# Optimization experiments

Measured on AMD Instinct MI355X. Metric: run time of the kernel, lower is better.

## Reference

```python
import jax, jax.numpy as jnp
from jax import lax
import numpy as np

N = 60000   # total nodes
B = 8       # graphs in batch
GS = N // B # nodes per graph
F = 384     # input node features
E = 600000  # edges
H = 6       # hiddenSize (hardcoded in source)
C = 10      # num_classes


def setup_inputs() -> dict:
    key = jax.random.key(0)
    ks = jax.random.split(key, 8)
    x = jax.random.normal(ks[0], (N, F), jnp.float32)
    src = jax.random.randint(ks[1], (E,), 0, N, jnp.int32)
    off = jax.random.randint(ks[2], (E,), 1, GS, jnp.int32)  # 1..GS-1 -> no self loops
    dst = (src // GS) * GS + (src % GS + off) % GS           # same-graph endpoint
    batch = jnp.arange(N, dtype=jnp.int32) // GS
    W1 = jax.random.normal(ks[3], (F, H), jnp.float32) * (1.0 / np.sqrt(F))
    b1 = jnp.zeros((H,), jnp.float32)
    W2 = jax.random.normal(ks[4], (H, C), jnp.float32) * (1.0 / np.sqrt(H))
    b2 = jnp.zeros((C,), jnp.float32)
    Wp1 = jax.random.normal(ks[5], (2 * H,), jnp.float32) * (1.0 / np.sqrt(2 * H))
    bp1 = jnp.zeros((), jnp.float32)
    Wp2 = jax.random.normal(ks[6], (2 * C,), jnp.float32) * (1.0 / np.sqrt(2 * C))
    bp2 = jnp.zeros((), jnp.float32)
    return dict(x=x, src=src, dst=dst, batch=batch, W1=W1, b1=b1, W2=W2, b2=b2,
                Wp1=Wp1, bp1=bp1, Wp2=Wp2, bp2=bp2)


def gcn_conv(x, src, dst, evalid, nvalid, W, b):
    # PyG GCNConv: h = x W; add remaining self-loops (weight 1); deg over dst;
    # norm = dinv[src]*dinv[dst]; aggregate to dst; + bias.
    n = x.shape[0]
    h = x @ W
    ef = evalid.astype(h.dtype)
    is_loop = evalid & (src == dst)
    has_loop = jax.ops.segment_sum(is_loop.astype(jnp.int32), dst, num_segments=n) > 0
    add_loop = (nvalid & ~has_loop).astype(h.dtype)
    deg = jax.ops.segment_sum(ef, dst, num_segments=n) + add_loop
    dinv = jnp.where(deg > 0, lax.rsqrt(jnp.maximum(deg, 1e-12)), 0.0)
    coef = ef * dinv[src] * dinv[dst]
    out = jax.ops.segment_sum(h[src] * coef[:, None], dst, num_segments=n)
    out = out + (add_loop * dinv * dinv)[:, None] * h
    return out + b


def edge_pool(x, src, dst, evalid, nvalid, Wp, bp):
    # PyG EdgePooling: raw = lin([x_src||x_dst]); score = softmax(raw, dst) + 0.5;
    # greedy contraction of edges by descending score; new_x = (sum over cluster) * score.
    n, f = x.shape
    raw = x[src] @ Wp[:f] + x[dst] @ Wp[f:] + bp                      # [E]
    rm = jnp.where(evalid, raw, -jnp.inf)
    m = jax.ops.segment_max(rm, dst, num_segments=n)
    m = jnp.where(jnp.isfinite(m), m, 0.0)
    ex = jnp.where(evalid, jnp.exp(raw - m[dst]), 0.0)
    s = jax.ops.segment_sum(ex, dst, num_segments=n)
    score = jnp.where(evalid, ex / jnp.where(s[dst] > 0, s[dst], 1.0), 0.0) + 0.5

    order = jnp.argsort(jnp.where(evalid, -score, jnp.inf))           # descending, invalid last

    def step(rem, edg):
        s_, d_, v_ = edg
        take = v_ & rem[s_] & rem[d_]
        rem = rem.at[s_].set(rem[s_] & ~take)
        rem = rem.at[d_].set(rem[d_] & ~take)
        return rem, take

    _, chosen_sorted = lax.scan(step, nvalid, (src[order], dst[order], evalid[order]))
    chosen = jnp.zeros_like(evalid).at[order].set(chosen_sorted)

    chf = chosen.astype(x.dtype)
    nonself = src != dst
    dead = jax.ops.segment_sum((chosen & nonself).astype(jnp.int32), dst, num_segments=n) > 0
    new_valid = nvalid & ~dead

    # merged feature: (x_src + x_dst) * score at slot src; unmatched: x * 1
    added = jnp.zeros_like(x).at[src].add((chf * nonself.astype(x.dtype))[:, None] * x[dst])
    scale = 1.0 + jnp.zeros((n,), x.dtype).at[src].add(chf * (score - 1.0))
    new_x = jnp.where(new_valid[:, None], (x + added) * scale[:, None], 0.0)

    # cluster map (dst of chosen edge -> src slot), remap + coalesce (dedup) edges
    merged_src = jnp.full((n,), -1, jnp.int32).at[dst].max(jnp.where(chosen, src, -1))
    cmap = jnp.where(merged_src >= 0, merged_src, jnp.arange(n, dtype=jnp.int32))
    ns, nd = cmap[src], cmap[dst]
    ns_k = jnp.where(evalid, ns, n)  # push invalid edges to the end
    order2 = jnp.lexsort((nd, ns_k))
    ss, dd = ns_k[order2], nd[order2]
    diff = (ss[1:] != ss[:-1]) | (dd[1:] != dd[:-1])
    first = jnp.concatenate([jnp.ones((1,), bool), diff])
    new_evalid = jnp.zeros_like(evalid).at[order2].set(first & evalid[order2])
    return new_x, ns, nd, new_evalid, new_valid


def _forward(x, src, dst, batch, W1, b1, W2, b2, Wp1, bp1, Wp2, bp2):
    evalid = jnp.ones((src.shape[0],), bool)
    nvalid = jnp.ones((x.shape[0],), bool)
    h = jax.nn.relu(gcn_conv(x, src, dst, evalid, nvalid, W1, b1))
    # dropout: identity in eval mode
    h, s1, d1, ev1, nv1 = edge_pool(h, src, dst, evalid, nvalid, Wp1, bp1)
    h = gcn_conv(h, s1, d1, ev1, nv1, W2, b2)
    h, s2, d2, ev2, nv2 = edge_pool(h, s1, d1, ev1, nv1, Wp2, bp2)
    nvf = nv2.astype(h.dtype)
    cnt = jax.ops.segment_sum(nvf, batch, num_segments=B)
    sm = jax.ops.segment_sum(h * nvf[:, None], batch, num_segments=B)
    g = sm / cnt[:, None]
    return jax.nn.log_softmax(g, axis=1)


def reference(x, src, dst, batch, W1, b1, W2, b2, Wp1, bp1, Wp2, bp2):
    return _forward(x, src, dst, batch, W1, b1, W2, b2, Wp1, bp1, Wp2, bp2)
```

## Files before the change

kernel.cpp:

```cpp
#include <hip/hip_runtime.h>
#include <math.h>

#define NN 60000
#define BB 8
#define GS 7500
#define FF 384
#define EE 600000
#define HH 6
#define CC 10
#define HT_BITS 20
#define HT_SIZE (1u << HT_BITS)
#define HT_MASK (HT_SIZE - 1u)
#define TPB 256
#define CAP 80000
#define REMW ((GS + 31) / 32)
#define GPAD 32
#define SCAN_B 1024
#define NBLK ((NN + SCAN_B - 1) / SCAN_B)
static_assert(NBLK <= 64, "scan3 wave-scan assumes <=64 blocks");
static_assert((HH % 2) == 0 && (CC % 2) == 0, "float2 paths assume even fd");

static inline int ngrid(int n) { return (n + TPB - 1) / TPB; }

__device__ __forceinline__ unsigned long long mkprio(float sc, int e) {
  return (((unsigned long long)__float_as_uint(sc)) << 32) |
         (unsigned int)(~(unsigned int)e);
}

__global__ void k_mm1(const float* __restrict__ x, const float* __restrict__ W,
                      float* __restrict__ out) {
  __shared__ float Ws[FF * HH];
  for (int i = threadIdx.x; i < FF * HH; i += blockDim.x) Ws[i] = W[i];
  __syncthreads();
  int wave = threadIdx.x >> 6, lane = threadIdx.x & 63;
  int node = blockIdx.x * 4 + wave;
  if (node >= NN) return;
  const float* xr = x + (size_t)node * FF;
  float acc[HH] = {0.f, 0.f, 0.f, 0.f, 0.f, 0.f};
  for (int k = lane; k < FF; k += 64) {
    float xv = xr[k];
#pragma unroll
    for (int j = 0; j < HH; j++) acc[j] += xv * Ws[k * HH + j];
  }
#pragma unroll
  for (int j = 0; j < HH; j++) {
#pragma unroll
    for (int o = 32; o > 0; o >>= 1) acc[j] += __shfl_down(acc[j], o, 64);
  }
  if (lane == 0) {
#pragma unroll
    for (int j = 0; j < HH; j++) out[(size_t)node * HH + j] = acc[j];
  }
}

__global__ void k_prep(float* __restrict__ deg, unsigned char* __restrict__ hasloop,
                       int* __restrict__ gcntsA,
                       int* __restrict__ gcntsB, float* __restrict__ gsum,
                       float* __restrict__ gcnt, const unsigned char* __restrict__ nvin,
                       unsigned char* __restrict__ nvout, float* __restrict__ scale,
                       int* __restrict__ merged, int* __restrict__ partner,
                       unsigned long long* __restrict__ bestA,
                       unsigned long long* __restrict__ bestB,
                       unsigned char* __restrict__ remG) {
  int v = blockIdx.x * blockDim.x + threadIdx.x;
  if (v >= NN) return;
  deg[v] = 0.f;
  hasloop[v] = 0;
  unsigned char nvv = nvin ? nvin[v] : 1;
  nvout[v] = nvv;
  remG[v] = nvv;
  bestA[v] = 0ULL;
  bestB[v] = 0ULL;
  scale[v] = 1.0f;
  if (merged) merged[v] = -1;
  partner[v] = -1;
  if (v < BB * GPAD) { gcntsA[v] = 0; gcntsB[v] = 0; }
  if (v < BB * CC) gsum[v] = 0.f;
  if (v < BB) gcnt[v] = 0.f;
}

__global__ void k_deg(const int* __restrict__ src, const int* __restrict__ dst,
                      const unsigned char* __restrict__ ev, float* __restrict__ deg,
                      unsigned char* __restrict__ hasloop) {
  int e = blockIdx.x * blockDim.x + threadIdx.x;
  if (e >= EE) return;
  if (ev && !ev[e]) return;
  int d = dst[e];
  atomicAdd(&deg[d], 1.0f);
  if (src[e] == d) hasloop[d] = 1;
}

__global__ __launch_bounds__(1024) void k_scan1(const float* __restrict__ deg,
                                                int* __restrict__ rowstart,
                                                int* __restrict__ bsum) {
  __shared__ int tmp[SCAN_B];
  int t = threadIdx.x;
  int i = blockIdx.x * SCAN_B + t;
  int v = (i < NN) ? (int)deg[i] : 0;
  tmp[t] = v;
  __syncthreads();
  for (int o = 1; o < SCAN_B; o <<= 1) {
    int y = (t >= o) ? tmp[t - o] : 0;
    __syncthreads();
    tmp[t] += y;
    __syncthreads();
  }
  if (i < NN) rowstart[i] = tmp[t] - v;
  if (t == SCAN_B - 1) bsum[blockIdx.x] = tmp[t];
}

__global__ void k_scan3(int* __restrict__ rowstart, const int* __restrict__ bsum,
                        int* __restrict__ fill, const float* __restrict__ deg,
                        const unsigned char* __restrict__ hasloop,
                        const unsigned char* __restrict__ nv, float* __restrict__ dinv,
                        unsigned char* __restrict__ addloop) {
  __shared__ int offs[64];
  __shared__ int total;
  int t = threadIdx.x;
  if (t < 64) {
    int v = (t < NBLK) ? bsum[t] : 0;
    int x = v;
#pragma unroll
    for (int o = 1; o < 64; o <<= 1) {
      int y = __shfl_up(x, o, 64);
      if (t >= o) x += y;
    }
    offs[t] = x - v;
    if (t == 63) total = x;
  }
  __syncthreads();
  int i = blockIdx.x * blockDim.x + t;
  if (i >= NN) return;
  int r = rowstart[i] + offs[i >> 10];
  rowstart[i] = r;
  fill[i] = r;
  if (i == NN - 1) rowstart[NN] = total;
  int nvv = nv ? (int)nv[i] : 1;
  unsigned char al = (nvv && !hasloop[i]) ? 1 : 0;
  float d = deg[i] + (float)al;
  dinv[i] = d > 0.f ? 1.0f / sqrtf(fmaxf(d, 1e-12f)) : 0.f;
  addloop[i] = al;
}

__global__ void k_scatter(const int* __restrict__ src, const int* __restrict__ dst,
                          const unsigned char* __restrict__ ev, int* __restrict__ fill,
                          int* __restrict__ csrS, int* __restrict__ csrE) {
  int e = blockIdx.x * blockDim.x + threadIdx.x;
  if (e >= EE) return;
  if (ev && !ev[e]) return;
  int d = dst[e];
  int p = atomicAdd(&fill[d], 1);
  csrS[p] = src[e];
  csrE[p] = e;
}

template <int FD>
__global__ void k_agg_fin(const int* __restrict__ rowstart, const int* __restrict__ csrS,
                          const float* __restrict__ dinv, const unsigned char* __restrict__ addloop,
                          const float* __restrict__ h, const float* __restrict__ b,
                          float* __restrict__ out, int relu) {
  int v = blockIdx.x * blockDim.x + threadIdx.x;
  if (v >= NN) return;
  int b0 = rowstart[v], b1 = rowstart[v + 1];
  float acc[FD];
#pragma unroll
  for (int j = 0; j < FD; j++) acc[j] = 0.f;
  float dv = dinv[v];
  for (int i = b0; i < b1; i++) {
    int s = csrS[i];
    float c = dinv[s] * dv;
    const float2* hr2 = (const float2*)(h + (size_t)s * FD);
#pragma unroll
    for (int j = 0; j < FD / 2; j++) {
      float2 hv = hr2[j];
      acc[2 * j] += hv.x * c;
      acc[2 * j + 1] += hv.y * c;
    }
  }
  float cl = addloop[v] ? dv * dv : 0.f;
  const float* hv = h + (size_t)v * FD;
#pragma unroll
  for (int j = 0; j < FD; j++) {
    float o = acc[j] + cl * hv[j] + b[j];
    if (relu) o = fmaxf(o, 0.f);
    out[(size_t)v * FD + j] = o;
  }
}

__global__ void k_raw(const float* __restrict__ x, const int* __restrict__ src,
                      const int* __restrict__ dst, const unsigned char* __restrict__ ev,
                      const float* __restrict__ Wp, const float* __restrict__ bp,
                      float* __restrict__ raw, unsigned char* __restrict__ chosen, int fd) {
  int e = blockIdx.x * blockDim.x + threadIdx.x;
  if (e >= EE) return;
  chosen[e] = 0;
  if (ev && !ev[e]) return;
  int s = src[e], d = dst[e];
  float r = bp[0];
  const float2* xs = (const float2*)(x + (size_t)s * fd);
  const float2* xd = (const float2*)(x + (size_t)d * fd);
  int h2 = fd >> 1;
  for (int j = 0; j < h2; j++) {
    float2 v = xs[j];
    r += v.x * Wp[2 * j];
    r += v.y * Wp[2 * j + 1];
  }
  for (int j = 0; j < h2; j++) {
    float2 v = xd[j];
    r += v.x * Wp[fd + 2 * j];
    r += v.y * Wp[fd + 2 * j + 1];
  }
  raw[e] = r;
}

__global__ void k_smscore(const int* __restrict__ rowstart, const int* __restrict__ csrS,
                          const int* __restrict__ csrE, const float* __restrict__ raw,
                          const unsigned char* __restrict__ remG, float* __restrict__ score,
                          unsigned long long* __restrict__ bestA) {
  int v = blockIdx.x * blockDim.x + threadIdx.x;
  if (v >= NN) return;
  int b0 = rowstart[v], b1 = rowstart[v + 1];
  if (b0 == b1) return;
  float m = -INFINITY;
  for (int i = b0; i < b1; i++) m = fmaxf(m, raw[csrE[i]]);
  float s = 0.f;
  for (int i = b0; i < b1; i++) s += expf(raw[csrE[i]] - m);
  if (!remG[v]) return;
  float sd = s > 0.f ? s : 1.0f;
  unsigned long long lb = 0ULL;
  for (int i = b0; i < b1; i++) {
    int sv = csrS[i];
    if (!remG[sv]) continue;
    int e = csrE[i];
    float sc = expf(raw[e] - m) / sd + 0.5f;
    score[e] = sc;
    unsigned long long p = mkprio(sc, e);
    if (p > lb) lb = p;
    if (sv != v && p > bestA[sv]) atomicMax(&bestA[sv], p);
  }
  if (lb > bestA[v]) atomicMax(&bestA[v], lb);
}

__global__ void k_r1sel(const int* __restrict__ src, const int* __restrict__ dst,
                        const float* __restrict__ score, const unsigned char* __restrict__ ev,
                        unsigned char* __restrict__ remG,
                        const unsigned long long* __restrict__ bestA,
                        unsigned long long* __restrict__ bestB,
                        unsigned char* __restrict__ chosen, ulonglong2* __restrict__ recs,
                        int* __restrict__ gcnts) {
  __shared__ int wcnt[TPB / 64][BB];
  __shared__ int bbase[BB];
  int e = blockIdx.x * blockDim.x + threadIdx.x;
  int w = threadIdx.x >> 6, lane = threadIdx.x & 63;
  int keep = 0, s = 0, d = 0, g = 0;
  unsigned long long p = 0;
  if (e < EE && (!ev || ev[e])) {
    s = src[e];
    d = dst[e];
    g = s / GS;
    if (remG[s] && remG[d]) {
      p = mkprio(score[e], e);
      if (bestA[s] == p && bestA[d] == p) {
        chosen[e] = 1;
        remG[s] = 0;
        remG[d] = 0;
      } else {
        keep = 1;
        bestB[s] = 0ULL;
        bestB[d] = 0ULL;
      }
    }
  }
  int myrank = 0;
#pragma unroll
  for (int gg = 0; gg < BB; gg++) {
    unsigned long long m = __ballot(keep && g == gg);
    if (keep && g == gg) myrank = __popcll(m & ((1ULL << lane) - 1ULL));
    if (lane == 0) wcnt[w][gg] = __popcll(m);
  }
  __syncthreads();
  if (threadIdx.x < BB) {
    int gg = threadIdx.x, tot = 0;
#pragma unroll
    for (int ww = 0; ww < TPB / 64; ww++) {
      int c = wcnt[ww][gg];
      wcnt[ww][gg] = tot;
      tot += c;
    }
    bbase[gg] = tot ? atomicAdd(&gcnts[gg * GPAD], tot) : 0;
  }
  __syncthreads();
  if (keep)
    recs[(size_t)g * CAP + bbase[g] + wcnt[w][g] + myrank] =
        make_ulonglong2(p, (((unsigned long long)(unsigned int)s) << 32) | (unsigned int)d);
}

__global__ void k_gpost(const ulonglong2* __restrict__ recs, const int* __restrict__ gcnts,
                        const unsigned char* __restrict__ remG,
                        unsigned long long* __restrict__ bestC, int* __restrict__ gcntsOut) {
  int g = blockIdx.y;
  if (blockIdx.x == 0 && threadIdx.x == 0) gcntsOut[g * GPAD] = 0;
  int n = gcnts[g * GPAD];
  const ulonglong2* lst = recs + (size_t)g * CAP;
  int stride = gridDim.x * blockDim.x;
  for (int i = blockIdx.x * blockDim.x + threadIdx.x; i < n; i += stride) {
    ulonglong2 r = lst[i];
    int s = (int)(r.y >> 32), d = (int)(r.y & 0xFFFFFFFFu);
    if (remG[s] && remG[d]) {
      if (r.x > bestC[s]) atomicMax(&bestC[s], r.x);
      if (d != s && r.x > bestC[d]) atomicMax(&bestC[d], r.x);
    }
  }
}

__global__ void k_gsel(const ulonglong2* __restrict__ recsIn, const int* __restrict__ gcntsIn,
                       unsigned char* __restrict__ remG,
                       const unsigned long long* __restrict__ bestC,
                       unsigned long long* __restrict__ bestN,
                       unsigned char* __restrict__ chosen, ulonglong2* __restrict__ recsOut,
                       int* __restrict__ gcntsOut) {
  int g = blockIdx.y;
  int n = gcntsIn[g * GPAD];
  const ulonglong2* lst = recsIn + (size_t)g * CAP;
  ulonglong2* outl = recsOut + (size_t)g * CAP;
  int lane = threadIdx.x & 63;
  int stride = gridDim.x * blockDim.x;
  for (int i = blockIdx.x * blockDim.x + threadIdx.x; i - lane < n; i += stride) {
    int keep = 0;
    ulonglong2 r;
    if (i < n) {
      r = lst[i];
      int s = (int)(r.y >> 32), d = (int)(r.y & 0xFFFFFFFFu);
      if (remG[s] && remG[d]) {
        if (bestC[s] == r.x && bestC[d] == r.x) {
          int e = (int)(~(unsigned int)(r.x & 0xFFFFFFFFu));
          chosen[e] = 1;
          remG[s] = 0;
          remG[d] = 0;
        } else {
          keep = 1;
          bestN[s] = 0ULL;
          bestN[d] = 0ULL;
        }
      }
    }
    unsigned long long m = __ballot(keep);
    int tot = __popcll(m);
    int pre = __popcll(m & ((1ULL << lane) - 1ULL));
    int b0 = 0;
    if (lane == 0 && tot) b0 = atomicAdd(&gcntsOut[g * GPAD], tot);
    b0 = __shfl(b0, 0, 64);
    if (keep) outl[b0 + pre] = r;
  }
}

__global__ __launch_bounds__(1024) void k_match_g(ulonglong2* __restrict__ recs0,
                                                  ulonglong2* __restrict__ recs1,
                                                  const int* __restrict__ gcnts,
                                                  const unsigned char* __restrict__ remG,
                                                  unsigned char* __restrict__ chosen) {
  __shared__ unsigned long long best[GS];
  __shared__ unsigned int remB[REMW];
  __shared__ int cnt_next;
  const int g = blockIdx.x;
  const int base = g * GS;
  const int t = threadIdx.x, nth = blockDim.x;
  const int lane = t & 63;

  for (int w = t; w < REMW; w += nth) {
    unsigned int bits = 0;
    int v0 = w * 32;
    if (v0 + 32 <= GS) {
      const unsigned int* p4 = (const unsigned int*)(remG + base + v0);
#pragma unroll
      for (int q = 0; q < 8; q++) {
        unsigned int x4 = p4[q];
        bits |= ((x4 & 1u) << (q * 4)) | (((x4 >> 8) & 1u) << (q * 4 + 1)) |
                (((x4 >> 16) & 1u) << (q * 4 + 2)) | (((x4 >> 24) & 1u) << (q * 4 + 3));
      }
    } else {
      for (int b = 0; b < 32; b++) {
        int v = v0 + b;
        if (v < GS) bits |= (remG[base + v] ? 1u : 0u) << b;
      }
    }
    remB[w] = bits;
  }
  for (int i = t; i < GS; i += nth) best[i] = 0ULL;
  __syncthreads();

  ulonglong2* bufs[2] = {recs0 + (size_t)g * CAP, recs1 + (size_t)g * CAP};
  int n = gcnts[g * GPAD];
  int cur = 0;
  int guard = 0;

  while (n > 0) {
    if (++guard > 100000) break;
    for (int i0 = 0; i0 < n; i0 += nth * 4) {
      ulonglong2 r[4];
      int have[4];
#pragma unroll
      for (int k = 0; k < 4; k++) {
        int i = i0 + t + k * nth;
        have[k] = i < n;
        if (have[k]) r[k] = bufs[cur][i];
      }
#pragma unroll
      for (int k = 0; k < 4; k++) {
        if (!have[k]) continue;
        int ls = (int)(r[k].y >> 32) - base, ld = (int)(r[k].y & 0xFFFFFFFFu) - base;
        if (((remB[ls >> 5] >> (ls & 31)) & 1u) && ((remB[ld >> 5] >> (ld & 31)) & 1u)) {
          atomicMax(&best[ls], r[k].x);
          if (ld != ls) atomicMax(&best[ld], r[k].x);
        }
      }
    }
    if (t == 0) cnt_next = 0;
    __syncthreads();
    for (int i0 = 0; i0 < n; i0 += nth * 4) {
      ulonglong2 r[4];
      int have[4];
#pragma unroll
      for (int k = 0; k < 4; k++) {
        int i = i0 + t + k * nth;
        have[k] = i < n;
        if (have[k]) r[k] = bufs[cur][i];
      }
#pragma unroll
      for (int k = 0; k < 4; k++) {
        int keep = 0;
        int ls = 0, ld = 0;
        if (have[k]) {
          ls = (int)(r[k].y >> 32) - base;
          ld = (int)(r[k].y & 0xFFFFFFFFu) - base;
          if (((remB[ls >> 5] >> (ls & 31)) & 1u) && ((remB[ld >> 5] >> (ld & 31)) & 1u)) {
            if (best[ls] == r[k].x && best[ld] == r[k].x) {
              int e = (int)(~(unsigned int)(r[k].x & 0xFFFFFFFFu));
              chosen[e] = 1;
              atomicAnd(&remB[ls >> 5], ~(1u << (ls & 31)));
              atomicAnd(&remB[ld >> 5], ~(1u << (ld & 31)));
            } else {
              keep = 1;
            }
          }
        }
        unsigned long long m = __ballot(keep);
        int tot = __popcll(m);
        int pre = __popcll(m & ((1ULL << lane) - 1ULL));
        int b0 = 0;
        if (lane == 0 && tot) b0 = atomicAdd(&cnt_next, tot);
        b0 = __shfl(b0, 0, 64);
        if (keep) bufs[cur ^ 1][b0 + pre] = r[k];
      }
    }
    __syncthreads();
    n = cnt_next;
    if (n < 4096) {
      for (int i = t; i < n; i += nth) {
        ulonglong2 r = bufs[cur ^ 1][i];
        best[(int)(r.y >> 32) - base] = 0ULL;
        best[(int)(r.y & 0xFFFFFFFFu) - base] = 0ULL;
      }
    } else {
      for (int i = t; i < GS; i += nth) best[i] = 0ULL;
    }
    __syncthreads();
    cur ^= 1;
  }
}

__global__ void k_pool_edge(const int* __restrict__ src, const int* __restrict__ dst,
                            const unsigned char* __restrict__ chosen, const float* __restrict__ score,
                            unsigned char* __restrict__ nvout, float* __restrict__ scale,
                            int* __restrict__ partner, int* __restrict__ merged) {
  int e = blockIdx.x * blockDim.x + threadIdx.x;
  if (e >= EE) return;
  if (!chosen[e]) return;
  int s = src[e], d = dst[e];
  scale[s] = score[e];
  if (merged) merged[d] = s;
  if (s != d) {
    nvout[d] = 0;
    partner[s] = d;
  }
}

__global__ void k_newx_mm2(const float* __restrict__ h1, const int* __restrict__ partner,
                           const float* __restrict__ scale, const unsigned char* __restrict__ nvout,
                           const float* __restrict__ W2, float* __restrict__ h2pre) {
  int v = blockIdx.x * blockDim.x + threadIdx.x;
  if (v >= NN) return;
  float sc = scale[v];
  int ok = nvout[v];
  int p = partner[v];
  float nx[HH];
#pragma unroll
  for (int j = 0; j < HH; j++) {
    float a = h1[(size_t)v * HH + j];
    if (p >= 0) a += h1[(size_t)p * HH + j];
    nx[j] = ok ? a * sc : 0.f;
  }
#pragma unroll
  for (int c = 0; c < CC; c++) {
    float a = 0.f;
#pragma unroll
    for (int j = 0; j < HH; j++) a += nx[j] * W2[j * CC + c];
    h2pre[(size_t)v * CC + c] = a;
  }
}

__device__ __forceinline__ unsigned int ht_hash(unsigned long long key) {
  return (unsigned int)((key * 0x9E3779B97F4A7C15ULL) >> 44) & HT_MASK;
}

__global__ void k_remap_ins(const int* __restrict__ src, const int* __restrict__ dst,
                            const int* __restrict__ merged, int* __restrict__ ns,
                            int* __restrict__ nd, unsigned long long* __restrict__ htab) {
  int e = blockIdx.x * blockDim.x + threadIdx.x;
  if (e >= EE) return;
  int s = src[e], d = dst[e];
  int ms = merged[s], md = merged[d];
  int a = ms >= 0 ? ms : s;
  int b = md >= 0 ? md : d;
  ns[e] = a;
  nd[e] = b;
  unsigned long long key =
      (unsigned long long)((((unsigned int)a) << 16) | (unsigned int)b);
  unsigned long long val = (key << 32) | (unsigned int)e;
  unsigned int h = ht_hash(key);
  for (;;) {
    unsigned long long curv = htab[h];
    if (curv == ~0ULL) {
      unsigned long long prev = atomicCAS(&htab[h], ~0ULL, val);
      if (prev == ~0ULL) break;
      curv = prev;
    }
    if ((curv >> 32) == key) {
      if ((curv & 0xFFFFFFFFULL) > (unsigned long long)(unsigned int)e)
        atomicMin(&htab[h], val);
      break;
    }
    h = (h + 1) & HT_MASK;
  }
}

__global__ void k_dedup_mark(const int* __restrict__ ns, const int* __restrict__ nd,
                             const unsigned long long* __restrict__ htab,
                             unsigned char* __restrict__ evout) {
  int e = blockIdx.x * blockDim.x + threadIdx.x;
  if (e >= EE) return;
  unsigned long long key =
      (unsigned long long)((((unsigned int)ns[e]) << 16) | (unsigned int)nd[e]);
  unsigned int h = ht_hash(key);
  for (;;) {
    unsigned long long curv = htab[h];
    if ((curv >> 32) == key) {
      evout[e] = ((curv & 0xFFFFFFFFULL) == (unsigned long long)(unsigned int)e) ? 1 : 0;
      return;
    }
    h = (h + 1) & HT_MASK;
  }
}

__global__ void k_newx_pool(const float* __restrict__ h2, const int* __restrict__ partner,
                            const float* __restrict__ scale, const unsigned char* __restrict__ nv,
                            float* __restrict__ gsum, float* __restrict__ gcnt) {
  int v = blockIdx.x * blockDim.x + threadIdx.x;
  int lane = threadIdx.x & 63;
  int b = (v < NN ? v : NN - 1) / GS;
  int active = (v < NN) && nv[v];
  float cnt = active ? 1.f : 0.f;
  float val[CC];
  if (active) {
    float sc = scale[v];
    int p = partner[v];
    for (int j = 0; j < CC; j++) {
      float a = h2[(size_t)v * CC + j];
      if (p >= 0) a += h2[(size_t)p * CC + j];
      val[j] = a * sc;
    }
  } else {
    for (int j = 0; j < CC; j++) val[j] = 0.f;
  }
  int b0 = __shfl(b, 0, 64);
  unsigned long long same = __ballot(b == b0);
  if (same == ~0ULL) {
    for (int o = 32; o > 0; o >>= 1) {
      cnt += __shfl_down(cnt, o, 64);
      for (int j = 0; j < CC; j++) val[j] += __shfl_down(val[j], o, 64);
    }
    if (lane == 0 && cnt > 0.f) {
      atomicAdd(&gcnt[b0], cnt);
      for (int j = 0; j < CC; j++) atomicAdd(&gsum[b0 * CC + j], val[j]);
    }
  } else if (active) {
    atomicAdd(&gcnt[b], cnt);
    for (int j = 0; j < CC; j++) atomicAdd(&gsum[b * CC + j], val[j]);
  }
}

__global__ void k_logsm(const float* __restrict__ gsum, const float* __restrict__ gcnt,
                        float* __restrict__ out) {
  int t = threadIdx.x;
  if (t >= BB) return;
  float gr[CC];
  float c = gcnt[t];
  float m = -INFINITY;
  for (int j = 0; j < CC; j++) {
    gr[j] = gsum[t * CC + j] / c;
    m = fmaxf(m, gr[j]);
  }
  float s = 0.f;
  for (int j = 0; j < CC; j++) s += expf(gr[j] - m);
  float l = logf(s);
  for (int j = 0; j < CC; j++) out[t * CC + j] = gr[j] - m - l;
}

extern "C" void kernel_launch(void* const* d_in, const int* in_sizes, int n_in,
                              void* d_out, int out_size, void* d_ws, size_t ws_size,
                              hipStream_t stream) {
  const float* x = (const float*)d_in[0];
  const int* src = (const int*)d_in[1];
  const int* dst = (const int*)d_in[2];
  const float* W1 = (const float*)d_in[4];
  const float* b1 = (const float*)d_in[5];
  const float* W2 = (const float*)d_in[6];
  const float* b2 = (const float*)d_in[7];
  const float* Wp1 = (const float*)d_in[8];
  const float* bp1 = (const float*)d_in[9];
  const float* Wp2 = (const float*)d_in[10];
  const float* bp2 = (const float*)d_in[11];
  float* out = (float*)d_out;

  char* wsb = (char*)d_ws;
  size_t off = 0;
  auto A = [&](size_t bytes) -> char* {
    char* r = wsb + off;
    off = (off + bytes + 255) & ~(size_t)255;
    return r;
  };
  float* h1pre = (float*)A((size_t)NN * HH * 4);
  float* h1out = (float*)A((size_t)NN * HH * 4);
  float* deg = (float*)A((size_t)NN * 4);
  float* dinv = (float*)A((size_t)NN * 4);
  unsigned char* hasloop = (unsigned char*)A(NN);
  unsigned char* addloop = (unsigned char*)A(NN);
  float* raw = (float*)A((size_t)EE * 4);
  float* score = (float*)A((size_t)EE * 4);
  unsigned char* chosen = (unsigned char*)A(EE);
  unsigned char* nv1 = (unsigned char*)A(NN);
  unsigned char* nv2 = (unsigned char*)A(NN);
  float* scale = (float*)A((size_t)NN * 4);
  int* partner = (int*)A((size_t)NN * 4);
  int* merged = (int*)A((size_t)NN * 4);
  int* ns = (int*)A((size_t)EE * 4);
  int* nd = (int*)A((size_t)EE * 4);
  unsigned char* ev1 = (unsigned char*)A(EE);
  unsigned long long* htab = (unsigned long long*)A((size_t)HT_SIZE * 8);
  float* h2pre = (float*)A((size_t)NN * CC * 4);
  float* h2out = (float*)A((size_t)NN * CC * 4);
  unsigned long long* bestA = (unsigned long long*)A((size_t)NN * 8);
  unsigned long long* bestB = (unsigned long long*)A((size_t)NN * 8);
  unsigned char* remG = (unsigned char*)A(NN);
  ulonglong2* recs0 = (ulonglong2*)A((size_t)BB * CAP * 16);
  ulonglong2* recs1 = (ulonglong2*)A((size_t)BB * CAP * 16);
  int* gcntsA = (int*)A((size_t)BB * GPAD * 4);
  int* gcntsB = (int*)A((size_t)BB * GPAD * 4);
  float* gsum = (float*)A((size_t)BB * CC * 4);
  float* gcnt = (float*)A((size_t)BB * 4);
  int* rowstart = (int*)A((size_t)(NN + 1) * 4);
  int* fill = (int*)A((size_t)NN * 4);
  int* bsum = (int*)A((size_t)64 * 4);
  int* csrS = (int*)A((size_t)EE * 4);
  int* csrE = (int*)A((size_t)EE * 4);
  (void)ws_size; (void)n_in; (void)in_sizes; (void)out_size;

  const int GE = ngrid(EE), GN = ngrid(NN);
  const dim3 RG(32, BB);

  hipMemsetAsync(htab, 0xFF, (size_t)HT_SIZE * 8, stream);
  hipLaunchKernelGGL(k_mm1, dim3((NN + 3) / 4), dim3(TPB), 0, stream, x, W1, h1pre);
  hipLaunchKernelGGL(k_prep, dim3(GN), dim3(TPB), 0, stream, deg, hasloop, gcntsA, gcntsB,
                     gsum, gcnt, (const unsigned char*)nullptr, nv1, scale, merged, partner, bestA, bestB, remG);
  hipLaunchKernelGGL(k_deg, dim3(GE), dim3(TPB), 0, stream, src, dst, (const unsigned char*)nullptr, deg, hasloop);
  hipLaunchKernelGGL(k_scan1, dim3(NBLK), dim3(SCAN_B), 0, stream, deg, rowstart, bsum);
  hipLaunchKernelGGL(k_scan3, dim3(GN), dim3(TPB), 0, stream, rowstart, bsum, fill, deg, hasloop,
                     (const unsigned char*)nullptr, dinv, addloop);
  hipLaunchKernelGGL(k_scatter, dim3(GE), dim3(TPB), 0, stream, src, dst, (const unsigned char*)nullptr, fill, csrS, csrE);
  hipLaunchKernelGGL(k_agg_fin<HH>, dim3(GN), dim3(TPB), 0, stream, rowstart, csrS, dinv, addloop, h1pre, b1, h1out, 1);

  hipLaunchKernelGGL(k_raw, dim3(GE), dim3(TPB), 0, stream, h1out, src, dst, (const unsigned char*)nullptr, Wp1, bp1, raw, chosen, HH);
  hipLaunchKernelGGL(k_smscore, dim3(GN), dim3(TPB), 0, stream, rowstart, csrS, csrE, raw, remG, score, bestA);
  hipLaunchKernelGGL(k_r1sel, dim3(GE), dim3(TPB), 0, stream, src, dst, score, (const unsigned char*)nullptr, remG, bestA, bestB, chosen, recs0, gcntsA);
  hipLaunchKernelGGL(k_gpost, RG, dim3(TPB), 0, stream, recs0, gcntsA, remG, bestB, gcntsB);
  hipLaunchKernelGGL(k_gsel, RG, dim3(TPB), 0, stream, recs0, gcntsA, remG, bestB, bestA, chosen, recs1, gcntsB);
  hipLaunchKernelGGL(k_gpost, RG, dim3(TPB), 0, stream, recs1, gcntsB, remG, bestA, gcntsA);
  hipLaunchKernelGGL(k_gsel, RG, dim3(TPB), 0, stream, recs1, gcntsB, remG, bestA, bestB, chosen, recs0, gcntsA);
  hipLaunchKernelGGL(k_gpost, RG, dim3(TPB), 0, stream, recs0, gcntsA, remG, bestB, gcntsB);
  hipLaunchKernelGGL(k_gsel, RG, dim3(TPB), 0, stream, recs0, gcntsA, remG, bestB, bestA, chosen, recs1, gcntsB);
  hipLaunchKernelGGL(k_gpost, RG, dim3(TPB), 0, stream, recs1, gcntsB, remG, bestA, gcntsA);
  hipLaunchKernelGGL(k_gsel, RG, dim3(TPB), 0, stream, recs1, gcntsB, remG, bestA, bestB, chosen, recs0, gcntsA);
  hipLaunchKernelGGL(k_gpost, RG, dim3(TPB), 0, stream, recs0, gcntsA, remG, bestB, gcntsB);
  hipLaunchKernelGGL(k_gsel, RG, dim3(TPB), 0, stream, recs0, gcntsA, remG, bestB, bestA, chosen, recs1, gcntsB);
  hipLaunchKernelGGL(k_match_g, dim3(BB), dim3(1024), 0, stream, recs1, recs0, gcntsB, remG, chosen);
  hipLaunchKernelGGL(k_pool_edge, dim3(GE), dim3(TPB), 0, stream, src, dst, chosen, score, nv1, scale, partner, merged);
  hipLaunchKernelGGL(k_newx_mm2, dim3(GN), dim3(TPB), 0, stream, h1out, partner, scale, nv1, W2, h2pre);
  hipLaunchKernelGGL(k_remap_ins, dim3(GE), dim3(TPB), 0, stream, src, dst, merged, ns, nd, htab);
  hipLaunchKernelGGL(k_dedup_mark, dim3(GE), dim3(TPB), 0, stream, ns, nd, htab, ev1);

  hipLaunchKernelGGL(k_prep, dim3(GN), dim3(TPB), 0, stream, deg, hasloop, gcntsA, gcntsB,
                     gsum, gcnt, (const unsigned char*)nv1, nv2, scale, (int*)nullptr, partner, bestA, bestB, remG);
  hipLaunchKernelGGL(k_deg, dim3(GE), dim3(TPB), 0, stream, ns, nd, (const unsigned char*)ev1, deg, hasloop);
  hipLaunchKernelGGL(k_scan1, dim3(NBLK), dim3(SCAN_B), 0, stream, deg, rowstart, bsum);
  hipLaunchKernelGGL(k_scan3, dim3(GN), dim3(TPB), 0, stream, rowstart, bsum, fill, deg, hasloop,
                     (const unsigned char*)nv1, dinv, addloop);
  hipLaunchKernelGGL(k_scatter, dim3(GE), dim3(TPB), 0, stream, ns, nd, (const unsigned char*)ev1, fill, csrS, csrE);
  hipLaunchKernelGGL(k_agg_fin<CC>, dim3(GN), dim3(TPB), 0, stream, rowstart, csrS, dinv, addloop, h2pre, b2, h2out, 0);

  hipLaunchKernelGGL(k_raw, dim3(GE), dim3(TPB), 0, stream, h2out, ns, nd, (const unsigned char*)ev1, Wp2, bp2, raw, chosen, CC);
  hipLaunchKernelGGL(k_smscore, dim3(GN), dim3(TPB), 0, stream, rowstart, csrS, csrE, raw, remG, score, bestA);
  hipLaunchKernelGGL(k_r1sel, dim3(GE), dim3(TPB), 0, stream, ns, nd, score, (const unsigned char*)ev1, remG, bestA, bestB, chosen, recs0, gcntsA);
  hipLaunchKernelGGL(k_gpost, RG, dim3(TPB), 0, stream, recs0, gcntsA, remG, bestB, gcntsB);
  hipLaunchKernelGGL(k_gsel, RG, dim3(TPB), 0, stream, recs0, gcntsA, remG, bestB, bestA, chosen, recs1, gcntsB);
  hipLaunchKernelGGL(k_gpost, RG, dim3(TPB), 0, stream, recs1, gcntsB, remG, bestA, gcntsA);
  hipLaunchKernelGGL(k_gsel, RG, dim3(TPB), 0, stream, recs1, gcntsB, remG, bestA, bestB, chosen, recs0, gcntsA);
  hipLaunchKernelGGL(k_gpost, RG, dim3(TPB), 0, stream, recs0, gcntsA, remG, bestB, gcntsB);
  hipLaunchKernelGGL(k_gsel, RG, dim3(TPB), 0, stream, recs0, gcntsA, remG, bestB, bestA, chosen, recs1, gcntsB);
  hipLaunchKernelGGL(k_gpost, RG, dim3(TPB), 0, stream, recs1, gcntsB, remG, bestA, gcntsA);
  hipLaunchKernelGGL(k_gsel, RG, dim3(TPB), 0, stream, recs1, gcntsB, remG, bestA, bestB, chosen, recs0, gcntsA);
  hipLaunchKernelGGL(k_gpost, RG, dim3(TPB), 0, stream, recs0, gcntsA, remG, bestB, gcntsB);
  hipLaunchKernelGGL(k_gsel, RG, dim3(TPB), 0, stream, recs0, gcntsA, remG, bestB, bestA, chosen, recs1, gcntsB);
  hipLaunchKernelGGL(k_match_g, dim3(BB), dim3(1024), 0, stream, recs1, recs0, gcntsB, remG, chosen);
  hipLaunchKernelGGL(k_pool_edge, dim3(GE), dim3(TPB), 0, stream, ns, nd, chosen, score, nv2, scale, partner, (int*)nullptr);

  hipLaunchKernelGGL(k_newx_pool, dim3(GN), dim3(TPB), 0, stream, h2out, partner, scale, nv2, gsum, gcnt);
  hipLaunchKernelGGL(k_logsm, dim3(1), dim3(64), 0, stream, gsum, gcnt, out);
}
```

Before: 1.404 ms.

## Fuse iterative matching rounds into one cooperative kernel with grid syncs

Replaces the ten alternating k_gpost/k_gsel launches per pooling stage with a single cooperative kernel. It runs five rounds and separates the atomicMax phase from the select/compact phase with grid.sync(). The aim is to remove the per-launch overhead and inter-kernel gaps of twenty small launches. In exchange it adds grid-wide barrier cost and requires the 256-block grid to be co-resident for the cooperative launch.

```diff
diff --git a/kernel.cpp b/kernel.cpp
--- a/kernel.cpp
+++ b/kernel.cpp
@@ -1,5 +1,8 @@
 #include <hip/hip_runtime.h>
+#include <hip/hip_cooperative_groups.h>
 #include <math.h>
+
+namespace cg = cooperative_groups;
 
 #define NN 60000
 #define BB 8
@@ -295,62 +298,68 @@
         make_ulonglong2(p, (((unsigned long long)(unsigned int)s) << 32) | (unsigned int)d);
 }
 
-__global__ void k_gpost(const ulonglong2* __restrict__ recs, const int* __restrict__ gcnts,
-                        const unsigned char* __restrict__ remG,
-                        unsigned long long* __restrict__ bestC, int* __restrict__ gcntsOut) {
-  int g = blockIdx.y;
-  if (blockIdx.x == 0 && threadIdx.x == 0) gcntsOut[g * GPAD] = 0;
-  int n = gcnts[g * GPAD];
-  const ulonglong2* lst = recs + (size_t)g * CAP;
-  int stride = gridDim.x * blockDim.x;
-  for (int i = blockIdx.x * blockDim.x + threadIdx.x; i < n; i += stride) {
-    ulonglong2 r = lst[i];
-    int s = (int)(r.y >> 32), d = (int)(r.y & 0xFFFFFFFFu);
-    if (remG[s] && remG[d]) {
-      if (r.x > bestC[s]) atomicMax(&bestC[s], r.x);
-      if (d != s && r.x > bestC[d]) atomicMax(&bestC[d], r.x);
-    }
-  }
-}
-
-__global__ void k_gsel(const ulonglong2* __restrict__ recsIn, const int* __restrict__ gcntsIn,
-                       unsigned char* __restrict__ remG,
-                       const unsigned long long* __restrict__ bestC,
-                       unsigned long long* __restrict__ bestN,
-                       unsigned char* __restrict__ chosen, ulonglong2* __restrict__ recsOut,
-                       int* __restrict__ gcntsOut) {
-  int g = blockIdx.y;
-  int n = gcntsIn[g * GPAD];
-  const ulonglong2* lst = recsIn + (size_t)g * CAP;
-  ulonglong2* outl = recsOut + (size_t)g * CAP;
-  int lane = threadIdx.x & 63;
-  int stride = gridDim.x * blockDim.x;
-  for (int i = blockIdx.x * blockDim.x + threadIdx.x; i - lane < n; i += stride) {
-    int keep = 0;
-    ulonglong2 r;
-    if (i < n) {
-      r = lst[i];
-      int s = (int)(r.y >> 32), d = (int)(r.y & 0xFFFFFFFFu);
+__global__ void k_grounds(ulonglong2* __restrict__ recs0, ulonglong2* __restrict__ recs1,
+                          int* __restrict__ gcA, int* __restrict__ gcB,
+                          unsigned char* __restrict__ remG,
+                          unsigned long long* __restrict__ bestA,
+                          unsigned long long* __restrict__ bestB,
+                          unsigned char* __restrict__ chosen, int nrounds) {
+  cg::grid_group grid = cg::this_grid();
+  const int g = blockIdx.y;
+  const int lane = threadIdx.x & 63;
+  const int stride = gridDim.x * blockDim.x;
+  ulonglong2* rin = recs0;
+  ulonglong2* rout = recs1;
+  int* cin = gcA;
+  int* cout = gcB;
+  unsigned long long* bcur = bestB;
+  unsigned long long* bnext = bestA;
+
+  for (int r = 0; r < nrounds; r++) {
+    if (blockIdx.x == 0 && threadIdx.x == 0) cout[g * GPAD] = 0;
+    int n = cin[g * GPAD];
+    const ulonglong2* lst = rin + (size_t)g * CAP;
+    for (int i = blockIdx.x * blockDim.x + threadIdx.x; i < n; i += stride) {
+      ulonglong2 rr = lst[i];
+      int s = (int)(rr.y >> 32), d = (int)(rr.y & 0xFFFFFFFFu);
       if (remG[s] && remG[d]) {
-        if (bestC[s] == r.x && bestC[d] == r.x) {
-          int e = (int)(~(unsigned int)(r.x & 0xFFFFFFFFu));
-          chosen[e] = 1;
-          remG[s] = 0;
-          remG[d] = 0;
-        } else {
-          keep = 1;
-          bestN[s] = 0ULL;
-          bestN[d] = 0ULL;
+        if (rr.x > bcur[s]) atomicMax(&bcur[s], rr.x);
+        if (d != s && rr.x > bcur[d]) atomicMax(&bcur[d], rr.x);
+      }
+    }
+    grid.sync();
+    ulonglong2* outl = rout + (size_t)g * CAP;
+    for (int i = blockIdx.x * blockDim.x + threadIdx.x; i - lane < n; i += stride) {
+      int keep = 0;
+      ulonglong2 rr;
+      if (i < n) {
+        rr = lst[i];
+        int s = (int)(rr.y >> 32), d = (int)(rr.y & 0xFFFFFFFFu);
+        if (remG[s] && remG[d]) {
+          if (bcur[s] == rr.x && bcur[d] == rr.x) {
+            int e = (int)(~(unsigned int)(rr.x & 0xFFFFFFFFu));
+            chosen[e] = 1;
+            remG[s] = 0;
+            remG[d] = 0;
+          } else {
+            keep = 1;
+            bnext[s] = 0ULL;
+            bnext[d] = 0ULL;
+          }
         }
       }
-    }
-    unsigned long long m = __ballot(keep);
-    int tot = __popcll(m);
-    int pre = __popcll(m & ((1ULL << lane) - 1ULL));
-    int b0 = 0;
-    if (lane == 0 && tot) b0 = atomicAdd(&gcntsOut[g * GPAD], tot);
-    b0 = __shfl(b0, 0, 64);
-    if (keep) outl[b0 + pre] = r;
+      unsigned long long m = __ballot(keep);
+      int tot = __popcll(m);
+      int pre = __popcll(m & ((1ULL << lane) - 1ULL));
+      int b0 = 0;
+      if (lane == 0 && tot) b0 = atomicAdd(&cout[g * GPAD], tot);
+      b0 = __shfl(b0, 0, 64);
+      if (keep) outl[b0 + pre] = rr;
+    }
+    grid.sync();
+    ulonglong2* tr = rin; rin = rout; rout = tr;
+    int* tc = cin; cin = cout; cout = tc;
+    unsigned long long* tb = bcur; bcur = bnext; bnext = tb;
   }
 }
 
@@ -677,6 +686,8 @@
 
   const int GE = ngrid(EE), GN = ngrid(NN);
   const dim3 RG(32, BB);
+  int nrounds = 5;
+  void* gargs[] = {&recs0, &recs1, &gcntsA, &gcntsB, &remG, &bestA, &bestB, &chosen, &nrounds};
 
   hipMemsetAsync(htab, 0xFF, (size_t)HT_SIZE * 8, stream);
   hipLaunchKernelGGL(k_mm1, dim3((NN + 3) / 4), dim3(TPB), 0, stream, x, W1, h1pre);
@@ -692,16 +703,7 @@
   hipLaunchKernelGGL(k_raw, dim3(GE), dim3(TPB), 0, stream, h1out, src, dst, (const unsigned char*)nullptr, Wp1, bp1, raw, chosen, HH);
   hipLaunchKernelGGL(k_smscore, dim3(GN), dim3(TPB), 0, stream, rowstart, csrS, csrE, raw, remG, score, bestA);
   hipLaunchKernelGGL(k_r1sel, dim3(GE), dim3(TPB), 0, stream, src, dst, score, (const unsigned char*)nullptr, remG, bestA, bestB, chosen, recs0, gcntsA);
-  hipLaunchKernelGGL(k_gpost, RG, dim3(TPB), 0, stream, recs0, gcntsA, remG, bestB, gcntsB);
-  hipLaunchKernelGGL(k_gsel, RG, dim3(TPB), 0, stream, recs0, gcntsA, remG, bestB, bestA, chosen, recs1, gcntsB);
-  hipLaunchKernelGGL(k_gpost, RG, dim3(TPB), 0, stream, recs1, gcntsB, remG, bestA, gcntsA);
-  hipLaunchKernelGGL(k_gsel, RG, dim3(TPB), 0, stream, recs1, gcntsB, remG, bestA, bestB, chosen, recs0, gcntsA);
-  hipLaunchKernelGGL(k_gpost, RG, dim3(TPB), 0, stream, recs0, gcntsA, remG, bestB, gcntsB);
-  hipLaunchKernelGGL(k_gsel, RG, dim3(TPB), 0, stream, recs0, gcntsA, remG, bestB, bestA, chosen, recs1, gcntsB);
-  hipLaunchKernelGGL(k_gpost, RG, dim3(TPB), 0, stream, recs1, gcntsB, remG, bestA, gcntsA);
-  hipLaunchKernelGGL(k_gsel, RG, dim3(TPB), 0, stream, recs1, gcntsB, remG, bestA, bestB, chosen, recs0, gcntsA);
-  hipLaunchKernelGGL(k_gpost, RG, dim3(TPB), 0, stream, recs0, gcntsA, remG, bestB, gcntsB);
-  hipLaunchKernelGGL(k_gsel, RG, dim3(TPB), 0, stream, recs0, gcntsA, remG, bestB, bestA, chosen, recs1, gcntsB);
+  hipLaunchCooperativeKernel((const void*)k_grounds, RG, dim3(TPB), gargs, 0, stream);
   hipLaunchKernelGGL(k_match_g, dim3(BB), dim3(1024), 0, stream, recs1, recs0, gcntsB, remG, chosen);
   hipLaunchKernelGGL(k_pool_edge, dim3(GE), dim3(TPB), 0, stream, src, dst, chosen, score, nv1, scale, partner, merged);
   hipLaunchKernelGGL(k_newx_mm2, dim3(GN), dim3(TPB), 0, stream, h1out, partner, scale, nv1, W2, h2pre);
@@ -720,16 +722,7 @@
   hipLaunchKernelGGL(k_raw, dim3(GE), dim3(TPB), 0, stream, h2out, ns, nd, (const unsigned char*)ev1, Wp2, bp2, raw, chosen, CC);
   hipLaunchKernelGGL(k_smscore, dim3(GN), dim3(TPB), 0, stream, rowstart, csrS, csrE, raw, remG, score, bestA);
   hipLaunchKernelGGL(k_r1sel, dim3(GE), dim3(TPB), 0, stream, ns, nd, score, (const unsigned char*)ev1, remG, bestA, bestB, chosen, recs0, gcntsA);
-  hipLaunchKernelGGL(k_gpost, RG, dim3(TPB), 0, stream, recs0, gcntsA, remG, bestB, gcntsB);
-  hipLaunchKernelGGL(k_gsel, RG, dim3(TPB), 0, stream, recs0, gcntsA, remG, bestB, bestA, chosen, recs1, gcntsB);
-  hipLaunchKernelGGL(k_gpost, RG, dim3(TPB), 0, stream, recs1, gcntsB, remG, bestA, gcntsA);
-  hipLaunchKernelGGL(k_gsel, RG, dim3(TPB), 0, stream, recs1, gcntsB, remG, bestA, bestB, chosen, recs0, gcntsA);
-  hipLaunchKernelGGL(k_gpost, RG, dim3(TPB), 0, stream, recs0, gcntsA, remG, bestB, gcntsB);
-  hipLaunchKernelGGL(k_gsel, RG, dim3(TPB), 0, stream, recs0, gcntsA, remG, bestB, bestA, chosen, recs1, gcntsB);
-  hipLaunchKernelGGL(k_gpost, RG, dim3(TPB), 0, stream, recs1, gcntsB, remG, bestA, gcntsA);
-  hipLaunchKernelGGL(k_gsel, RG, dim3(TPB), 0, stream, recs1, gcntsB, remG, bestA, bestB, chosen, recs0, gcntsA);
-  hipLaunchKernelGGL(k_gpost, RG, dim3(TPB), 0, stream, recs0, gcntsA, remG, bestB, gcntsB);
-  hipLaunchKernelGGL(k_gsel, RG, dim3(TPB), 0, stream, recs0, gcntsA, remG, bestB, bestA, chosen, recs1, gcntsB);
+  hipLaunchCooperativeKernel((const void*)k_grounds, RG, dim3(TPB), gargs, 0, stream);
   hipLaunchKernelGGL(k_match_g, dim3(BB), dim3(1024), 0, stream, recs1, recs0, gcntsB, remG, chosen);
   hipLaunchKernelGGL(k_pool_edge, dim3(GE), dim3(TPB), 0, stream, ns, nd, chosen, score, nv2, scale, partner, (int*)nullptr);
 
```

Result: slower. 2.052 ms (+46.2%).
